# Optimization experiments

Measured on AMD Instinct MI355X. Metric: run time of the kernel, lower is better.

Reference implementation:

```python
import jax, jax.numpy as jnp
import numpy as np
import math

HEADS = 8

def setup_inputs() -> dict:
    key = jax.random.key(0)
    ks = jax.random.split(key, 7)
    b, n, e_n, H = 1, 10000, 32, 256
    q = jax.random.normal(ks[0], (b, n, H), dtype=jnp.float32)
    k = jax.random.normal(ks[1], (b, n, e_n, H + 3), dtype=jnp.float32)
    v = jax.random.normal(ks[2], (b, n, e_n, H + 3), dtype=jnp.float32)
    # Linear weights in torch convention: [out_features, in_features], no bias.
    Wq = jax.random.normal(ks[3], (H, H), dtype=jnp.float32) * (1.0 / math.sqrt(H))
    Wk = jax.random.normal(ks[4], (H, H + 3), dtype=jnp.float32) * (1.0 / math.sqrt(H + 3))
    Wv = jax.random.normal(ks[5], (H, H + 3), dtype=jnp.float32) * (1.0 / math.sqrt(H + 3))
    Wo = jax.random.normal(ks[6], (H, H), dtype=jnp.float32) * (1.0 / math.sqrt(H))
    return {"q": q, "k": k, "v": v, "Wq": Wq, "Wk": Wk, "Wv": Wv, "Wo": Wo}

def reference(q, k, v, Wq, Wk, Wv, Wo):
    b, n, e_n, _ = k.shape
    D = Wq.shape[0]               # heads * att_size
    d = D // HEADS                # att_size
    kp = jnp.einsum('bnec,dc->bned', k, Wk).reshape(b, n, e_n, HEADS, d)
    vp = jnp.einsum('bnec,dc->bned', v, Wv).reshape(b, n, e_n, HEADS, d)
    qp = jnp.einsum('bnc,dc->bnd', q, Wq).reshape(b, n, 1, HEADS, d)
    # per-neighbor dot product attention over neighbor axis e_n
    simi = jnp.sum(kp * qp, axis=-1) / jnp.sqrt(jnp.float32(d))  # (b,n,e_n,heads)
    att = jax.nn.softmax(simi, axis=2)
    out = jnp.sum(vp * att[..., None], axis=2)  # (b,n,heads,d)
    out = out.reshape(b, n, D)
    return jnp.einsum('bnd,od->bno', out, Wo)
```

## Files before the change

### kernel.cpp

```cpp
#include <hip/hip_runtime.h>
#include <hip/hip_bf16.h>

namespace {

constexpr int H      = 256;
constexpr int C      = 259;
constexpr int CP     = 260;
constexpr int E      = 32;
constexpr int NHEAD  = 8;
constexpr int NB     = 4;
constexpr float SCALE = 0.17677669529663687f;

__global__ __launch_bounds__(256, 4) void mha_neigh_kernel(
    const float* __restrict__ q, const float* __restrict__ kk, const float* __restrict__ vv,
    const float* __restrict__ Wq, const float* __restrict__ Wk,
    const float* __restrict__ Wv, const float* __restrict__ Wo,
    float* __restrict__ outp, int n)
{
    __shared__ __align__(16) float w_lds[NB * NHEAD * CP];
    __shared__ __align__(16) float uni[NB * 256];

    const int t  = threadIdx.x;
    const int n0 = blockIdx.x * NB;

    int node[NB];
    #pragma unroll
    for (int nb = 0; nb < NB; ++nb) {
        int nn = n0 + nb;
        node[nb] = (nn < n) ? nn : (n - 1);
    }

    {
        float acc[NB] = {};
        const float4* Wq4 = (const float4*)Wq;
        for (int i = 0; i < 64; ++i) {
            float4 wq = Wq4[t * 64 + i];
            #pragma unroll
            for (int nb = 0; nb < NB; ++nb) {
                float4 qv = *(const float4*)(q + (size_t)node[nb] * H + 4 * i);
                acc[nb] += wq.x * qv.x + wq.y * qv.y + wq.z * qv.z + wq.w * qv.w;
            }
        }
        #pragma unroll
        for (int nb = 0; nb < NB; ++nb) uni[nb * 256 + t] = acc[nb];
    }
    __syncthreads();

    {
        const int h  = t >> 5;
        const int c0 = t & 31;
        float acc[9 * NB] = {};
        for (int d = 0; d < 32; ++d) {
            const float* wkrow = Wk + (size_t)(h * 32 + d) * C;
            float qpv[NB];
            #pragma unroll
            for (int nb = 0; nb < NB; ++nb) qpv[nb] = uni[nb * 256 + h * 32 + d];
            #pragma unroll
            for (int j = 0; j < 9; ++j) {
                int c = c0 + 32 * j;
                if (c < C) {
                    float wkv = wkrow[c];
                    #pragma unroll
                    for (int nb = 0; nb < NB; ++nb) acc[j * NB + nb] += wkv * qpv[nb];
                }
            }
        }
        #pragma unroll
        for (int j = 0; j < 9; ++j) {
            int c = c0 + 32 * j;
            if (c < C) {
                #pragma unroll
                for (int nb = 0; nb < NB; ++nb) w_lds[(nb * NHEAD + h) * CP + c] = acc[j * NB + nb];
            }
        }
    }
    __syncthreads();

    {
        const int e = t >> 3;
        const int j = t & 7;
        #pragma unroll 1
        for (int nb = 0; nb < NB; ++nb) {
            const float* krow = kk + (size_t)node[nb] * (E * C) + (size_t)e * C;
            float acc[NHEAD] = {};
            #pragma unroll
            for (int m = 0; m < 8; ++m) {
                float4 k4 = *(const float4*)&krow[j * 4 + 32 * m];
                const float* wb = &w_lds[(nb * NHEAD) * CP + j * 4 + 32 * m];
                #pragma unroll
                for (int h = 0; h < NHEAD; ++h) {
                    float4 w4 = *(const float4*)&wb[h * CP];
                    acc[h] += k4.x * w4.x + k4.y * w4.y + k4.z * w4.z + k4.w * w4.w;
                }
            }
            if (j == 0) {
                #pragma unroll
                for (int ct = 0; ct < 3; ++ct) {
                    float kx = krow[256 + ct];
                    #pragma unroll
                    for (int h = 0; h < NHEAD; ++h)
                        acc[h] += kx * w_lds[(nb * NHEAD + h) * CP + 256 + ct];
                }
            }
            #pragma unroll
            for (int h = 0; h < NHEAD; ++h) {
                float s = acc[h];
                s += __shfl_xor(s, 1, 64);
                s += __shfl_xor(s, 2, 64);
                s += __shfl_xor(s, 4, 64);
                acc[h] = s;
            }
            float myv = 0.0f;
            #pragma unroll
            for (int h = 0; h < NHEAD; ++h) myv = (j == h) ? acc[h] : myv;
            uni[nb * 256 + e * 8 + j] = myv * SCALE;
        }
    }
    __syncthreads();

    {
        const int h   = t >> 5;
        const int e32 = t & 31;
        #pragma unroll
        for (int nb = 0; nb < NB; ++nb) {
            float s = uni[nb * 256 + e32 * 8 + h];
            float mx = s;
            #pragma unroll
            for (int off = 16; off >= 1; off >>= 1) mx = fmaxf(mx, __shfl_xor(mx, off, 64));
            float p = __expf(s - mx);
            float sum = p;
            #pragma unroll
            for (int off = 16; off >= 1; off >>= 1) sum += __shfl_xor(sum, off, 64);
            uni[nb * 256 + e32 * 8 + h] = p / sum;
        }
    }
    __syncthreads();

    {
        #pragma unroll 1
        for (int nb = 0; nb < NB; ++nb) {
            const float* vrow = vv + (size_t)node[nb] * (E * C);
            float acc[NHEAD] = {};
            for (int e = 0; e < E; ++e) {
                const float4* a4 = (const float4*)&uni[nb * 256 + e * 8];
                float4 a0 = a4[0];
                float4 a1 = a4[1];
                float x = vrow[e * C + t];
                acc[0] += a0.x * x; acc[1] += a0.y * x; acc[2] += a0.z * x; acc[3] += a0.w * x;
                acc[4] += a1.x * x; acc[5] += a1.y * x; acc[6] += a1.z * x; acc[7] += a1.w * x;
            }
            #pragma unroll
            for (int h = 0; h < NHEAD; ++h) w_lds[(nb * NHEAD + h) * CP + t] = acc[h];
            if (t < 3) {
                float a2[NHEAD] = {};
                for (int e = 0; e < E; ++e) {
                    const float4* a4 = (const float4*)&uni[nb * 256 + e * 8];
                    float4 a0 = a4[0];
                    float4 a1 = a4[1];
                    float x2 = vrow[e * C + 256 + t];
                    a2[0] += a0.x * x2; a2[1] += a0.y * x2; a2[2] += a0.z * x2; a2[3] += a0.w * x2;
                    a2[4] += a1.x * x2; a2[5] += a1.y * x2; a2[6] += a1.z * x2; a2[7] += a1.w * x2;
                }
                #pragma unroll
                for (int h = 0; h < NHEAD; ++h) w_lds[(nb * NHEAD + h) * CP + 256 + t] = a2[h];
            }
        }
    }
    __syncthreads();

    {
        const int h = t >> 5;
        const float* wvrow = Wv + (size_t)t * C;
        float acc[NB] = {};
        for (int c4 = 0; c4 < 64; ++c4) {
            float w0 = wvrow[4 * c4 + 0];
            float w1 = wvrow[4 * c4 + 1];
            float w2 = wvrow[4 * c4 + 2];
            float w3 = wvrow[4 * c4 + 3];
            #pragma unroll
            for (int nb = 0; nb < NB; ++nb) {
                float4 vb = *(const float4*)&w_lds[(nb * NHEAD + h) * CP + 4 * c4];
                acc[nb] += w0 * vb.x + w1 * vb.y + w2 * vb.z + w3 * vb.w;
            }
        }
        #pragma unroll
        for (int c = 256; c < 259; ++c) {
            float wvv = wvrow[c];
            #pragma unroll
            for (int nb = 0; nb < NB; ++nb) acc[nb] += wvv * w_lds[(nb * NHEAD + h) * CP + c];
        }
        #pragma unroll
        for (int nb = 0; nb < NB; ++nb) uni[nb * 256 + t] = acc[nb];
    }
    __syncthreads();

    {
        float acc[NB] = {};
        const float4* Wo4 = (const float4*)Wo;
        for (int i = 0; i < 64; ++i) {
            float4 wo = Wo4[t * 64 + i];
            #pragma unroll
            for (int nb = 0; nb < NB; ++nb) {
                float4 o4 = *(const float4*)&uni[nb * 256 + 4 * i];
                acc[nb] += wo.x * o4.x + wo.y * o4.y + wo.z * o4.z + wo.w * o4.w;
            }
        }
        #pragma unroll
        for (int nb = 0; nb < NB; ++nb) {
            if (n0 + nb < n) outp[(size_t)(n0 + nb) * H + t] = acc[nb];
        }
    }
}

}

extern "C" void kernel_launch(void* const* d_in, const int* in_sizes, int n_in,
                              void* d_out, int out_size, void* d_ws, size_t ws_size,
                              hipStream_t stream) {
    const float* q  = (const float*)d_in[0];
    const float* k  = (const float*)d_in[1];
    const float* v  = (const float*)d_in[2];
    const float* Wq = (const float*)d_in[3];
    const float* Wk = (const float*)d_in[4];
    const float* Wv = (const float*)d_in[5];
    const float* Wo = (const float*)d_in[6];
    float* out = (float*)d_out;

    const int n = in_sizes[0] / H;
    const int blocks = (n + NB - 1) / NB;

    mha_neigh_kernel<<<dim3(blocks), dim3(256), 0, stream>>>(
        q, k, v, Wq, Wk, Wv, Wo, out, n);
}
```

Before: 373.0 us.

## Coalesce weight-matrix GEMV loads with 8-lane row groups and shuffle reductions

Restructures the Wq, Wv and Wo projection stages so that each group of 8 lanes cooperatively reads one weight row with contiguous float4 loads, then reduces the partial sums with shuffles. Previously each thread walked its own row, which gave strided, uncoalesced global accesses. q is also staged in LDS first instead of being re-read from global memory. A few loop-unroll pragmas are added in the K and V stages. The cost is extra shuffle reductions and an additional barrier.

```diff
diff --git a/kernel.cpp b/kernel.cpp
--- a/kernel.cpp
+++ b/kernel.cpp
@@ -10,6 +10,10 @@
 constexpr int NHEAD  = 8;
 constexpr int NB     = 4;
 constexpr float SCALE = 0.17677669529663687f;
+
+__device__ __forceinline__ float dot4(float4 a, float4 b) {
+    return a.x * b.x + a.y * b.y + a.z * b.z + a.w * b.w;
+}
 
 __global__ __launch_bounds__(256, 4) void mha_neigh_kernel(
     const float* __restrict__ q, const float* __restrict__ kk, const float* __restrict__ vv,
@@ -20,8 +24,12 @@
     __shared__ __align__(16) float w_lds[NB * NHEAD * CP];
     __shared__ __align__(16) float uni[NB * 256];
 
-    const int t  = threadIdx.x;
-    const int n0 = blockIdx.x * NB;
+    const int t    = threadIdx.x;
+    const int wv   = t >> 6;
+    const int lane = t & 63;
+    const int dr   = lane >> 3;
+    const int cs   = lane & 7;
+    const int n0   = blockIdx.x * NB;
 
     int node[NB];
     #pragma unroll
@@ -30,19 +38,33 @@
         node[nb] = (nn < n) ? nn : (n - 1);
     }
 
-    {
-        float acc[NB] = {};
-        const float4* Wq4 = (const float4*)Wq;
-        for (int i = 0; i < 64; ++i) {
-            float4 wq = Wq4[t * 64 + i];
-            #pragma unroll
-            for (int nb = 0; nb < NB; ++nb) {
-                float4 qv = *(const float4*)(q + (size_t)node[nb] * H + 4 * i);
-                acc[nb] += wq.x * qv.x + wq.y * qv.y + wq.z * qv.z + wq.w * qv.w;
-            }
-        }
-        #pragma unroll
-        for (int nb = 0; nb < NB; ++nb) uni[nb * 256 + t] = acc[nb];
+    float* q_st = w_lds;
+    #pragma unroll
+    for (int nb = 0; nb < NB; ++nb) q_st[nb * 256 + t] = q[(size_t)node[nb] * H + t];
+    __syncthreads();
+
+    #pragma unroll
+    for (int p = 0; p < 8; ++p) {
+        const int row = p * 32 + wv * 8 + dr;
+        const float* wqrow = Wq + (size_t)row * H;
+        float a0 = 0.f, a1 = 0.f, a2 = 0.f, a3 = 0.f;
+        #pragma unroll
+        for (int m = 0; m < 8; ++m) {
+            float4 wq = *(const float4*)&wqrow[cs * 4 + 32 * m];
+            a0 += dot4(wq, *(const float4*)&q_st[0 * 256 + cs * 4 + 32 * m]);
+            a1 += dot4(wq, *(const float4*)&q_st[1 * 256 + cs * 4 + 32 * m]);
+            a2 += dot4(wq, *(const float4*)&q_st[2 * 256 + cs * 4 + 32 * m]);
+            a3 += dot4(wq, *(const float4*)&q_st[3 * 256 + cs * 4 + 32 * m]);
+        }
+        #pragma unroll
+        for (int off = 1; off <= 4; off <<= 1) {
+            a0 += __shfl_xor(a0, off, 64);
+            a1 += __shfl_xor(a1, off, 64);
+            a2 += __shfl_xor(a2, off, 64);
+            a3 += __shfl_xor(a3, off, 64);
+        }
+        float val = (cs == 0) ? a0 : (cs == 1) ? a1 : (cs == 2) ? a2 : a3;
+        if (cs < 4) uni[cs * 256 + row] = val;
     }
     __syncthreads();
 
@@ -79,7 +101,7 @@
     {
         const int e = t >> 3;
         const int j = t & 7;
-        #pragma unroll 1
+        #pragma unroll 2
         for (int nb = 0; nb < NB; ++nb) {
             const float* krow = kk + (size_t)node[nb] * (E * C) + (size_t)e * C;
             float acc[NHEAD] = {};
@@ -90,7 +112,7 @@
                 #pragma unroll
                 for (int h = 0; h < NHEAD; ++h) {
                     float4 w4 = *(const float4*)&wb[h * CP];
-                    acc[h] += k4.x * w4.x + k4.y * w4.y + k4.z * w4.z + k4.w * w4.w;
+                    acc[h] += dot4(k4, w4);
                 }
             }
             if (j == 0) {
@@ -141,6 +163,7 @@
         for (int nb = 0; nb < NB; ++nb) {
             const float* vrow = vv + (size_t)node[nb] * (E * C);
             float acc[NHEAD] = {};
+            #pragma unroll 8
             for (int e = 0; e < E; ++e) {
                 const float4* a4 = (const float4*)&uni[nb * 256 + e * 8];
                 float4 a0 = a4[0];
@@ -168,47 +191,64 @@
     }
     __syncthreads();
 
-    {
-        const int h = t >> 5;
-        const float* wvrow = Wv + (size_t)t * C;
-        float acc[NB] = {};
-        for (int c4 = 0; c4 < 64; ++c4) {
-            float w0 = wvrow[4 * c4 + 0];
-            float w1 = wvrow[4 * c4 + 1];
-            float w2 = wvrow[4 * c4 + 2];
-            float w3 = wvrow[4 * c4 + 3];
-            #pragma unroll
-            for (int nb = 0; nb < NB; ++nb) {
-                float4 vb = *(const float4*)&w_lds[(nb * NHEAD + h) * CP + 4 * c4];
-                acc[nb] += w0 * vb.x + w1 * vb.y + w2 * vb.z + w3 * vb.w;
-            }
-        }
-        #pragma unroll
-        for (int c = 256; c < 259; ++c) {
-            float wvv = wvrow[c];
-            #pragma unroll
-            for (int nb = 0; nb < NB; ++nb) acc[nb] += wvv * w_lds[(nb * NHEAD + h) * CP + c];
-        }
-        #pragma unroll
-        for (int nb = 0; nb < NB; ++nb) uni[nb * 256 + t] = acc[nb];
-    }
-    __syncthreads();
-
-    {
-        float acc[NB] = {};
-        const float4* Wo4 = (const float4*)Wo;
-        for (int i = 0; i < 64; ++i) {
-            float4 wo = Wo4[t * 64 + i];
-            #pragma unroll
-            for (int nb = 0; nb < NB; ++nb) {
-                float4 o4 = *(const float4*)&uni[nb * 256 + 4 * i];
-                acc[nb] += wo.x * o4.x + wo.y * o4.y + wo.z * o4.z + wo.w * o4.w;
-            }
-        }
-        #pragma unroll
-        for (int nb = 0; nb < NB; ++nb) {
-            if (n0 + nb < n) outp[(size_t)(n0 + nb) * H + t] = acc[nb];
-        }
+    #pragma unroll
+    for (int p = 0; p < 8; ++p) {
+        const int row = p * 32 + wv * 8 + dr;
+        const int h   = p;
+        const float* wvrow = Wv + (size_t)row * C;
+        float a0 = 0.f, a1 = 0.f, a2 = 0.f, a3 = 0.f;
+        #pragma unroll
+        for (int m = 0; m < 8; ++m) {
+            float4 wv4 = *(const float4*)&wvrow[cs * 4 + 32 * m];
+            a0 += dot4(wv4, *(const float4*)&w_lds[(0 * NHEAD + h) * CP + cs * 4 + 32 * m]);
+            a1 += dot4(wv4, *(const float4*)&w_lds[(1 * NHEAD + h) * CP + cs * 4 + 32 * m]);
+            a2 += dot4(wv4, *(const float4*)&w_lds[(2 * NHEAD + h) * CP + cs * 4 + 32 * m]);
+            a3 += dot4(wv4, *(const float4*)&w_lds[(3 * NHEAD + h) * CP + cs * 4 + 32 * m]);
+        }
+        if (cs == 0) {
+            #pragma unroll
+            for (int ct = 0; ct < 3; ++ct) {
+                float wvv = wvrow[256 + ct];
+                a0 += wvv * w_lds[(0 * NHEAD + h) * CP + 256 + ct];
+                a1 += wvv * w_lds[(1 * NHEAD + h) * CP + 256 + ct];
+                a2 += wvv * w_lds[(2 * NHEAD + h) * CP + 256 + ct];
+                a3 += wvv * w_lds[(3 * NHEAD + h) * CP + 256 + ct];
+            }
+        }
+        #pragma unroll
+        for (int off = 1; off <= 4; off <<= 1) {
+            a0 += __shfl_xor(a0, off, 64);
+            a1 += __shfl_xor(a1, off, 64);
+            a2 += __shfl_xor(a2, off, 64);
+            a3 += __shfl_xor(a3, off, 64);
+        }
+        float val = (cs == 0) ? a0 : (cs == 1) ? a1 : (cs == 2) ? a2 : a3;
+        if (cs < 4) uni[cs * 256 + row] = val;
+    }
+    __syncthreads();
+
+    #pragma unroll
+    for (int p = 0; p < 8; ++p) {
+        const int row = p * 32 + wv * 8 + dr;
+        const float* worow = Wo + (size_t)row * H;
+        float a0 = 0.f, a1 = 0.f, a2 = 0.f, a3 = 0.f;
+        #pragma unroll
+        for (int m = 0; m < 8; ++m) {
+            float4 wo = *(const float4*)&worow[cs * 4 + 32 * m];
+            a0 += dot4(wo, *(const float4*)&uni[0 * 256 + cs * 4 + 32 * m]);
+            a1 += dot4(wo, *(const float4*)&uni[1 * 256 + cs * 4 + 32 * m]);
+            a2 += dot4(wo, *(const float4*)&uni[2 * 256 + cs * 4 + 32 * m]);
+            a3 += dot4(wo, *(const float4*)&uni[3 * 256 + cs * 4 + 32 * m]);
+        }
+        #pragma unroll
+        for (int off = 1; off <= 4; off <<= 1) {
+            a0 += __shfl_xor(a0, off, 64);
+            a1 += __shfl_xor(a1, off, 64);
+            a2 += __shfl_xor(a2, off, 64);
+            a3 += __shfl_xor(a3, off, 64);
+        }
+        float val = (cs == 0) ? a0 : (cs == 1) ? a1 : (cs == 2) ? a2 : a3;
+        if (cs < 4 && (n0 + cs) < n) outp[(size_t)(n0 + cs) * H + row] = val;
     }
 }
 
```

Measured after the change: 305.5 us. -18.1%, faster.
